# Optimization experiments

Measured on AMD Instinct MI355X. Metric: run time of the kernel, lower is better.

## Reference

```python
import jax, jax.numpy as jnp
import numpy as np

B, Himg, Wimg, C, NH = 16, 64, 64, 256, 8
HD = C // NH  # 32
N = Himg * Wimg  # 4096


def _rotations(h, w, hd):
    # RMT/RAVLT 2D axial RoPE: head_dim split into two halves (rows, cols),
    # each half holds k_max = hd//4 complex frequencies.
    k_max = hd // 4
    theta = 1.0 / (10000.0 ** (np.arange(k_max) / k_max))
    ang_h = np.arange(h)[:, None] * theta  # (h, k_max)
    ang_w = np.arange(w)[:, None] * theta  # (w, k_max)
    ang = np.concatenate([
        np.broadcast_to(ang_h[:, None, :], (h, w, k_max)),
        np.broadcast_to(ang_w[None, :, :], (h, w, k_max)),
    ], axis=-1)  # (h, w, hd//2)
    return jnp.asarray(np.cos(ang), jnp.float32), jnp.asarray(np.sin(ang), jnp.float32)

COS, SIN = _rotations(Himg, Wimg, HD)


def _rope(x):
    # x: (b, nh, H, W, hd); complex rotation of (even, odd) channel pairs
    xr, xi = x[..., 0::2], x[..., 1::2]
    out_r = xr * COS - xi * SIN
    out_i = xr * SIN + xi * COS
    return jnp.stack([out_r, out_i], axis=-1).reshape(x.shape)


def setup_inputs() -> dict:
    key = jax.random.key(0)
    ks = jax.random.split(key, 5)
    return {
        "x": jax.random.normal(ks[0], (B, N, C), jnp.float32),
        "w_qkvo": jax.random.normal(ks[1], (C, 4 * C), jnp.float32) * 0.02,
        "b_qkvo": jnp.zeros((4 * C,), jnp.float32),
        "lepe_w": jax.random.normal(ks[2], (C, 1, 5, 5), jnp.float32) * 0.02,
        "lepe_b": jnp.zeros((C,), jnp.float32),
        "w_proj": jax.random.normal(ks[3], (C, C), jnp.float32) * 0.02,
        "b_proj": jnp.zeros((C,), jnp.float32),
    }


def reference(x, w_qkvo, b_qkvo, lepe_w, lepe_b, w_proj, b_proj):
    b, n, c = x.shape
    scale = HD ** -0.5
    qkvo = x @ w_qkvo + b_qkvo  # (b, n, 4c)
    q, k, v, o = (qkvo[..., i * c:(i + 1) * c] for i in range(4))
    # LePE: depthwise 5x5 conv on v viewed as an image
    v_img = v.reshape(b, Himg, Wimg, c).transpose(0, 3, 1, 2)  # NCHW
    lepe = jax.lax.conv_general_dilated(
        v_img, lepe_w, window_strides=(1, 1), padding=[(2, 2), (2, 2)],
        dimension_numbers=("NCHW", "OIHW", "NCHW"), feature_group_count=c,
    ) + lepe_b[None, :, None, None]
    # ELU+1 feature map
    q = jax.nn.elu(q) + 1.0
    k = jax.nn.elu(k) + 1.0
    q = q.reshape(b, n, NH, HD).transpose(0, 2, 1, 3)  # (b, nh, n, hd)
    k = k.reshape(b, n, NH, HD).transpose(0, 2, 1, 3)
    v = v.reshape(b, n, NH, HD).transpose(0, 2, 1, 3)
    # efficiency reweighting of keys
    q_mean = q.mean(axis=-2, keepdims=True)  # (b, nh, 1, hd)
    eff = jax.nn.softmax(scale * jnp.einsum("bhod,bhnd->bhon", q_mean, k), axis=-1)
    k = k * eff.transpose(0, 1, 3, 2) * n  # (b, nh, n, hd)
    # RoPE on q and reweighted k
    q_rope = _rope(q.reshape(b, NH, Himg, Wimg, HD)).reshape(b, NH, n, HD)
    k_rope = _rope(k.reshape(b, NH, Himg, Wimg, HD)).reshape(b, NH, n, HD)
    # normalizer from non-rope q and mean of reweighted k
    z = 1.0 / (jnp.einsum("bhnd,bhod->bhno", q, k.mean(axis=-2, keepdims=True)) + 1e-6)
    # linear attention: kv accumulation then q @ kv (scale n^-1 split as n^-0.5 each)
    inv_sqrt_n = n ** -0.5
    kv = jnp.einsum("bhnd,bhne->bhde", k_rope * inv_sqrt_n, v * inv_sqrt_n)  # (b, nh, hd, hd)
    out = jnp.einsum("bhnd,bhde->bhne", q_rope, kv) * z
    out = out.transpose(0, 2, 1, 3).reshape(b, n, c)
    out = out + lepe.transpose(0, 2, 3, 1).reshape(b, n, c)
    out = out * o  # gate
    return out @ w_proj + b_proj
```

## Files before the change

### kernel.cpp

```cpp
#include <hip/hip_runtime.h>
#include <math.h>

constexpr int B   = 16;
constexpr int IH  = 64;
constexpr int IW  = 64;
constexpr int C   = 256;
constexpr int NH  = 8;
constexpr int HD  = 32;
constexpr int N   = IH * IW;
constexpr int C4  = 4 * C;

using f16x8 = __attribute__((ext_vector_type(8))) _Float16;
using f32x4 = __attribute__((ext_vector_type(4))) float;

__global__ void k_tables(float* __restrict__ cosT, float* __restrict__ sinT) {
  int t = blockIdx.x * 256 + threadIdx.x;
  int j = t & 15, pix = t >> 4;
  int y = pix >> 6, x = pix & 63;
  int jj = j & 7;
  double theta = pow(10000.0, -(double)jj / 8.0);
  double pos = (j < 8) ? (double)y : (double)x;
  double ang = pos * theta;
  cosT[t] = (float)cos(ang);
  sinT[t] = (float)sin(ang);
}

__global__ void k_split_wT(const float* __restrict__ w, int ldb,
                           _Float16* __restrict__ hiT, _Float16* __restrict__ loT) {
  int n = blockIdx.x;
  int k = threadIdx.x;
  float v = w[(size_t)k * ldb + n];
  _Float16 h = (_Float16)v;
  hiT[(size_t)n * 256 + k] = h;
  loT[(size_t)n * 256 + k] = (_Float16)(v - (float)h);
}

__global__ __launch_bounds__(256) void k_gemm_split(
    const float* __restrict__ A, int lda,
    const _Float16* __restrict__ BhT, const _Float16* __restrict__ BlT,
    const float* __restrict__ bias, float* __restrict__ Cm, int ldc,
    int nelu, float* __restrict__ qpart) {
  __shared__ _Float16 lds[4 * 5120];
  _Float16* AhL = lds;
  _Float16* AlL = lds + 5120;
  _Float16* BhL = lds + 10240;
  _Float16* BlL = lds + 15360;
  int t = threadIdx.x;
  int m0 = blockIdx.x * 128, n0 = blockIdx.y * 128;
  int lane = t & 63;
  int wm = t >> 7, wn = (t >> 6) & 1;
  int lr = lane & 15, lg = lane >> 4;
  int srow = t >> 1, sseg = t & 1;

  f32x4 acc[4][4] = {};

  const float* aP = &A[(size_t)(m0 + srow) * lda + sseg * 16];
  const _Float16* bhP = &BhT[(size_t)(n0 + srow) * 256 + sseg * 16];
  const _Float16* blP = &BlT[(size_t)(n0 + srow) * 256 + sseg * 16];
  float4 ar0 = *(const float4*)(aP + 0);
  float4 ar1 = *(const float4*)(aP + 4);
  float4 ar2 = *(const float4*)(aP + 8);
  float4 ar3 = *(const float4*)(aP + 12);
  f16x8 brh0 = *(const f16x8*)(bhP + 0);
  f16x8 brh1 = *(const f16x8*)(bhP + 8);
  f16x8 brl0 = *(const f16x8*)(blP + 0);
  f16x8 brl1 = *(const f16x8*)(blP + 8);

  for (int kc = 0; kc < 256; kc += 32) {
    {
      float av[16] = {ar0.x, ar0.y, ar0.z, ar0.w, ar1.x, ar1.y, ar1.z, ar1.w,
                      ar2.x, ar2.y, ar2.z, ar2.w, ar3.x, ar3.y, ar3.z, ar3.w};
      f16x8 h0, h1, l0, l1;
#pragma unroll
      for (int j = 0; j < 8; ++j) {
        _Float16 h = (_Float16)av[j];
        h0[j] = h; l0[j] = (_Float16)(av[j] - (float)h);
        _Float16 h2 = (_Float16)av[j + 8];
        h1[j] = h2; l1[j] = (_Float16)(av[j + 8] - (float)h2);
      }
      int d = srow * 40 + sseg * 16;
      *(f16x8*)&AhL[d] = h0; *(f16x8*)&AhL[d + 8] = h1;
      *(f16x8*)&AlL[d] = l0; *(f16x8*)&AlL[d + 8] = l1;
      *(f16x8*)&BhL[d] = brh0; *(f16x8*)&BhL[d + 8] = brh1;
      *(f16x8*)&BlL[d] = brl0; *(f16x8*)&BlL[d + 8] = brl1;
    }
    __syncthreads();

    if (kc + 32 < 256) {
      const float* aN = aP + kc + 32;
      const _Float16* bhN = bhP + kc + 32;
      const _Float16* blN = blP + kc + 32;
      ar0 = *(const float4*)(aN + 0);
      ar1 = *(const float4*)(aN + 4);
      ar2 = *(const float4*)(aN + 8);
      ar3 = *(const float4*)(aN + 12);
      brh0 = *(const f16x8*)(bhN + 0);
      brh1 = *(const f16x8*)(bhN + 8);
      brl0 = *(const f16x8*)(blN + 0);
      brl1 = *(const f16x8*)(blN + 8);
    }

    f16x8 ah[4], al[4];
#pragma unroll
    for (int mi = 0; mi < 4; ++mi) {
      int ar = (wm * 64 + mi * 16 + lr) * 40 + lg * 8;
      ah[mi] = *(const f16x8*)&AhL[ar];
      al[mi] = *(const f16x8*)&AlL[ar];
    }
#pragma unroll
    for (int ni = 0; ni < 4; ++ni) {
      int br = (wn * 64 + ni * 16 + lr) * 40 + lg * 8;
      f16x8 bh = *(const f16x8*)&BhL[br];
      f16x8 bl = *(const f16x8*)&BlL[br];
#pragma unroll
      for (int mi = 0; mi < 4; ++mi) {
        acc[mi][ni] = __builtin_amdgcn_mfma_f32_16x16x32_f16(ah[mi], bh, acc[mi][ni], 0, 0, 0);
        acc[mi][ni] = __builtin_amdgcn_mfma_f32_16x16x32_f16(al[mi], bh, acc[mi][ni], 0, 0, 0);
        acc[mi][ni] = __builtin_amdgcn_mfma_f32_16x16x32_f16(ah[mi], bl, acc[mi][ni], 0, 0, 0);
      }
    }
    __syncthreads();
  }

  float* Cl = reinterpret_cast<float*>(lds);
  int ri2 = t >> 3, c0 = (t & 7) << 4;
  bool doq = (qpart != nullptr) && (n0 < 256);
  float qs[16] = {};
#pragma unroll
  for (int mi = 0; mi < 4; ++mi) {
#pragma unroll
    for (int ni = 0; ni < 4; ++ni) {
      int col = wn * 64 + ni * 16 + lr;
#pragma unroll
      for (int r = 0; r < 4; ++r)
        Cl[(wm * 16 + lg * 4 + r) * 132 + col] = acc[mi][ni][r];
    }
    __syncthreads();
    int grow = m0 + (ri2 >> 4) * 64 + mi * 16 + (ri2 & 15);
#pragma unroll
    for (int j = 0; j < 4; ++j) {
      int col = n0 + c0 + j * 4;
      float4 v = *(const float4*)&Cl[ri2 * 132 + c0 + j * 4];
      float4 bb = *(const float4*)&bias[col];
      v.x += bb.x; v.y += bb.y; v.z += bb.z; v.w += bb.w;
      if (col < nelu) {
        v.x = (v.x > 0.f) ? v.x + 1.f : expf(v.x);
        v.y = (v.y > 0.f) ? v.y + 1.f : expf(v.y);
        v.z = (v.z > 0.f) ? v.z + 1.f : expf(v.z);
        v.w = (v.w > 0.f) ? v.w + 1.f : expf(v.w);
      }
      if (doq) {
        qs[j * 4 + 0] += v.x; qs[j * 4 + 1] += v.y;
        qs[j * 4 + 2] += v.z; qs[j * 4 + 3] += v.w;
      }
      *(float4*)&Cm[(size_t)grow * ldc + col] = v;
    }
    __syncthreads();
  }
  if (doq) {
#pragma unroll
    for (int j = 0; j < 4; ++j) {
      float4 w4 = {qs[j*4+0], qs[j*4+1], qs[j*4+2], qs[j*4+3]};
      *(float4*)&Cl[ri2 * 132 + c0 + j * 4] = w4;
    }
    __syncthreads();
    if (t < 128) {
      float ssum = 0.f;
#pragma unroll
      for (int rr = 0; rr < 32; ++rr) ssum += Cl[rr * 132 + t];
      int b_local = m0 >> 12, rowblk = (m0 >> 7) & 31;
      qpart[(size_t)(b_local * 32 + rowblk) * 256 + n0 + t] = ssum;
    }
  }
}

__global__ __launch_bounds__(256) void k_kvflash(
    const float* __restrict__ qkvo, const float* __restrict__ qpart,
    const float* __restrict__ cosT, const float* __restrict__ sinT,
    float* __restrict__ kvp) {
  __shared__ float qm[32];
  __shared__ float sL[512];
  __shared__ float red[256];
  __shared__ float ktG[4][32][36];
  __shared__ float vtG[4][32][36];
  int bh = blockIdx.x, chunk = blockIdx.y;
  int b = bh >> 3, h = bh & 7;
  int t = threadIdx.x;
  int nbase = chunk << 9;

  if (t < 32) {
    float s = 0.f;
#pragma unroll
    for (int rb = 0; rb < 32; ++rb)
      s += qpart[(size_t)(b * 32 + rb) * 256 + (h << 5) + t];
    qm[t] = s * (1.0f / N) * 0.1767766952966369f;
  }
  __syncthreads();

  float qmr[32];
#pragma unroll
  for (int i = 0; i < 32; ++i) qmr[i] = qm[i];
  float mx = -3.4e38f;
#pragma unroll
  for (int i = 0; i < 2; ++i) {
    int n = nbase + t + i * 256;
    const float* kp = &qkvo[(size_t)(b * N + n) * C4 + 256 + (h << 5)];
    float dot = 0.f;
#pragma unroll
    for (int j = 0; j < 8; ++j) {
      float4 k4 = *(const float4*)(kp + (j << 2));
      dot += k4.x * qmr[j*4] + k4.y * qmr[j*4+1] + k4.z * qmr[j*4+2] + k4.w * qmr[j*4+3];
    }
    sL[t + i * 256] = dot;
    mx = fmaxf(mx, dot);
  }
  red[t] = mx; __syncthreads();
  for (int off = 128; off > 0; off >>= 1) {
    if (t < off) red[t] = fmaxf(red[t], red[t + off]);
    __syncthreads();
  }
  float mx_c = red[0];
  __syncthreads();
  float psum = expf(sL[t] - mx_c) + expf(sL[t + 256] - mx_c);
  red[t] = psum; __syncthreads();
  for (int off = 128; off > 0; off >>= 1) {
    if (t < off) red[t] += red[t + off];
    __syncthreads();
  }
  float sum_c = red[0];

  int sg = t >> 6;
  int lane = t & 63;
  int d0 = (lane >> 3) << 2;
  int e0 = (lane & 7) << 2;
  int srow_l = (t >> 1) & 31;
  int sdh = t & 1;
  float acc[4][4] = {};
  float km16[16] = {};

  for (int s = 0; s < 4; ++s) {
    int nloc = sg * 128 + s * 32 + srow_l;
    int n = nbase + nloc;
    const float* kp = &qkvo[(size_t)(b * N + n) * C4 + 256 + (h << 5) + sdh * 16];
    const float* vp = kp + 256;
    float ef = expf(sL[nloc] - mx_c);
    float kl[16], vl[16];
#pragma unroll
    for (int j4 = 0; j4 < 4; ++j4) {
      float4 k4 = *(const float4*)(kp + (j4 << 2));
      float4 v4 = *(const float4*)(vp + (j4 << 2));
      k4.x *= ef; k4.y *= ef; k4.z *= ef; k4.w *= ef;
      km16[j4*4+0] += k4.x; km16[j4*4+1] += k4.y;
      km16[j4*4+2] += k4.z; km16[j4*4+3] += k4.w;
      kl[j4*4+0] = k4.x; kl[j4*4+1] = k4.y; kl[j4*4+2] = k4.z; kl[j4*4+3] = k4.w;
      vl[j4*4+0] = v4.x; vl[j4*4+1] = v4.y; vl[j4*4+2] = v4.z; vl[j4*4+3] = v4.w;
    }
#pragma unroll
    for (int p = 0; p < 8; ++p) {
      float cc = cosT[(n << 4) + sdh * 8 + p];
      float sn = sinT[(n << 4) + sdh * 8 + p];
      float kr = kl[2*p], ki = kl[2*p+1];
      kl[2*p]   = kr * cc - ki * sn;
      kl[2*p+1] = kr * sn + ki * cc;
    }
#pragma unroll
    for (int j4 = 0; j4 < 4; ++j4) {
      float4 kw = {kl[j4*4+0], kl[j4*4+1], kl[j4*4+2], kl[j4*4+3]};
      float4 vw = {vl[j4*4+0], vl[j4*4+1], vl[j4*4+2], vl[j4*4+3]};
      *(float4*)&ktG[sg][srow_l][sdh*16 + (j4 << 2)] = kw;
      *(float4*)&vtG[sg][srow_l][sdh*16 + (j4 << 2)] = vw;
    }
    __syncthreads();
    __builtin_amdgcn_s_setprio(1);
#pragma unroll
    for (int nn = 0; nn < 32; ++nn) {
      float4 k4 = *(const float4*)&ktG[sg][nn][d0];
      float4 v4 = *(const float4*)&vtG[sg][nn][e0];
      float kv_[4] = {k4.x, k4.y, k4.z, k4.w};
      float vv_[4] = {v4.x, v4.y, v4.z, v4.w};
#pragma unroll
      for (int i = 0; i < 4; ++i)
#pragma unroll
        for (int j = 0; j < 4; ++j)
          acc[i][j] = fmaf(kv_[i], vv_[j], acc[i][j]);
    }
    __builtin_amdgcn_s_setprio(0);
    __syncthreads();
  }

  float* mrg = &ktG[0][0][0];
#pragma unroll
  for (int i = 0; i < 4; ++i)
#pragma unroll
    for (int j = 0; j < 4; ++j)
      mrg[sg * 1024 + (d0 + i) * 32 + (e0 + j)] = acc[i][j];
  __syncthreads();
  size_t o = (size_t)(bh * 8 + chunk) * 1058;
  {
    int idx = t << 2;
    float4 r;
    r.x = mrg[idx+0] + mrg[1024+idx+0] + mrg[2048+idx+0] + mrg[3072+idx+0];
    r.y = mrg[idx+1] + mrg[1024+idx+1] + mrg[2048+idx+1] + mrg[3072+idx+1];
    r.z = mrg[idx+2] + mrg[1024+idx+2] + mrg[2048+idx+2] + mrg[3072+idx+2];
    r.w = mrg[idx+3] + mrg[1024+idx+3] + mrg[2048+idx+3] + mrg[3072+idx+3];
    kvp[o + idx + 0] = r.x; kvp[o + idx + 1] = r.y;
    kvp[o + idx + 2] = r.z; kvp[o + idx + 3] = r.w;
  }
  float* kmb = &vtG[0][0][0];
#pragma unroll
  for (int j = 0; j < 16; ++j) kmb[t * 16 + j] = km16[j];
  __syncthreads();
  if (t < 32) {
    int dh = t >> 4, dj = t & 15;
    float ssum = 0.f;
    for (int r = 0; r < 128; ++r) ssum += kmb[((r << 1) + dh) * 16 + dj];
    kvp[o + 1024 + t] = ssum;
  }
  if (t == 0) {
    kvp[o + 1056] = mx_c;
    kvp[o + 1057] = sum_c;
  }
}

__global__ __launch_bounds__(256) void k_kvfinal(
    const float* __restrict__ kvp, float* __restrict__ kvkm) {
  __shared__ float fc[8];
  int bh = blockIdx.x;
  int t = threadIdx.x;
  if (t == 0) {
    float mxs[8], sums[8];
    float mx = -3.4e38f;
#pragma unroll
    for (int c = 0; c < 8; ++c) {
      size_t o = (size_t)(bh * 8 + c) * 1058;
      mxs[c] = kvp[o + 1056];
      sums[c] = kvp[o + 1057];
      mx = fmaxf(mx, mxs[c]);
    }
    float T = 0.f;
#pragma unroll
    for (int c = 0; c < 8; ++c) T += sums[c] * expf(mxs[c] - mx);
    float invT = 1.0f / T;
#pragma unroll
    for (int c = 0; c < 8; ++c) fc[c] = expf(mxs[c] - mx) * invT;
  }
  __syncthreads();
  float f0 = fc[0], f1 = fc[1], f2 = fc[2], f3 = fc[3];
  float f4 = fc[4], f5 = fc[5], f6 = fc[6], f7 = fc[7];
  for (int j = t; j < 1056; j += 256) {
    size_t o = (size_t)(bh * 8) * 1058 + j;
    float v = kvp[o] * f0 + kvp[o + 1058] * f1 + kvp[o + 2 * 1058] * f2 +
              kvp[o + 3 * 1058] * f3 + kvp[o + 4 * 1058] * f4 +
              kvp[o + 5 * 1058] * f5 + kvp[o + 6 * 1058] * f6 +
              kvp[o + 7 * 1058] * f7;
    kvkm[(size_t)bh * 1056 + j] = v;
  }
}

__global__ __launch_bounds__(256) void k_lepe(
    const float* __restrict__ qkvo, const float* __restrict__ wgt,
    const float* __restrict__ lb, float* __restrict__ lepe_out, int b0) {
  int blk = blockIdx.x;
  int b = blk >> 8, rem = blk & 255;
  int y = rem >> 2, x0 = (rem & 3) << 4;
  int c = threadIdx.x;
  float w[25];
#pragma unroll
  for (int i = 0; i < 25; ++i) w[i] = wgt[c * 25 + i];
  float bias = lb[c];
  float acc[16];
#pragma unroll
  for (int p = 0; p < 16; ++p) acc[p] = bias;
#pragma unroll
  for (int dy = 0; dy < 5; ++dy) {
    int yy = y + dy - 2;
    if (yy < 0 || yy >= IH) continue;
    size_t rowb = (size_t)(b * N + (yy << 6)) * C4 + 512 + c;
#pragma unroll
    for (int dx = 0; dx < 5; ++dx) {
      float wv = w[dy * 5 + dx];
#pragma unroll
      for (int p = 0; p < 16; ++p) {
        int xx = x0 + p + dx - 2;
        if (xx < 0 || xx >= IW) continue;
        acc[p] = fmaf(qkvo[rowb + (size_t)xx * C4], wv, acc[p]);
      }
    }
  }
#pragma unroll
  for (int p = 0; p < 16; ++p)
    lepe_out[(size_t)((b0 + b) * N + (y << 6) + x0 + p) * C + c] = acc[p];
}

__global__ __launch_bounds__(256) void k_out_combine(
    float* __restrict__ qkvo, const float* __restrict__ kvkm,
    const float* __restrict__ cosT, const float* __restrict__ sinT,
    const float* __restrict__ lepe, int b0) {
  __shared__ float kvs[1024];
  __shared__ float kms[32];
  int bh = blockIdx.x, chunk = blockIdx.y;
  int b = bh >> 3, h = bh & 7;
  int t = threadIdx.x;
  reinterpret_cast<float4*>(kvs)[t] =
      reinterpret_cast<const float4*>(&kvkm[(size_t)bh * 1056])[t];
  if (t < 32) kms[t] = kvkm[(size_t)bh * 1056 + 1024 + t];
  __syncthreads();
  int n = (chunk << 8) + t;
  size_t rowbase = (size_t)(b * N + n) * C4;
  float q[32];
#pragma unroll
  for (int i = 0; i < 8; ++i) {
    float4 q4 = *reinterpret_cast<const float4*>(&qkvo[rowbase + (h << 5) + (i << 2)]);
    q[i * 4 + 0] = q4.x; q[i * 4 + 1] = q4.y; q[i * 4 + 2] = q4.z; q[i * 4 + 3] = q4.w;
  }
  float dot = 0.f;
#pragma unroll
  for (int dd = 0; dd < 32; ++dd) dot += q[dd] * kms[dd];
  float zv = 1.0f / (dot + 1e-6f);
  const float* cp = &cosT[n << 4];
  const float* sp = &sinT[n << 4];
#pragma unroll
  for (int j = 0; j < 16; ++j) {
    float cc = cp[j], ss = sp[j];
    float qr = q[2 * j], qi = q[2 * j + 1];
    q[2 * j]     = qr * cc - qi * ss;
    q[2 * j + 1] = qr * ss + qi * cc;
  }
  size_t oc = (size_t)((b0 + b) * N + n) * C + (h << 5);
#pragma unroll
  for (int e4 = 0; e4 < 8; ++e4) {
    float ax = 0, ay = 0, az = 0, aw = 0;
#pragma unroll
    for (int dd = 0; dd < 32; ++dd) {
      float4 kv4 = *reinterpret_cast<const float4*>(&kvs[(dd << 5) + (e4 << 2)]);
      float qd = q[dd];
      ax = fmaf(qd, kv4.x, ax); ay = fmaf(qd, kv4.y, ay);
      az = fmaf(qd, kv4.z, az); aw = fmaf(qd, kv4.w, aw);
    }
    float4 lp = *reinterpret_cast<const float4*>(&lepe[oc + (e4 << 2)]);
    float4 ov = *reinterpret_cast<const float4*>(
        &qkvo[rowbase + 768 + (h << 5) + (e4 << 2)]);
    float4 r;
    r.x = (ax * zv + lp.x) * ov.x;
    r.y = (ay * zv + lp.y) * ov.y;
    r.z = (az * zv + lp.z) * ov.z;
    r.w = (aw * zv + lp.w) * ov.w;
    *reinterpret_cast<float4*>(&qkvo[rowbase + (h << 5) + (e4 << 2)]) = r;
  }
}

static inline size_t ws_bytes_needed(int bpp) {
  size_t pn = (size_t)bpp * N;
  size_t f32c = pn * C4
              + (size_t)bpp * 32 * 256
              + (size_t)bpp * NH * 8 * 1058
              + (size_t)bpp * NH * 1056
              + (size_t)N * 16 * 2;
  size_t f16c = (size_t)C * C4 * 2
              + (size_t)C * C * 2;
  return f32c * 4 + f16c * 2;
}

extern "C" void kernel_launch(void* const* d_in, const int* in_sizes, int n_in,
                              void* d_out, int out_size, void* d_ws, size_t ws_size,
                              hipStream_t stream) {
  const float* x      = (const float*)d_in[0];
  const float* w_qkvo = (const float*)d_in[1];
  const float* b_qkvo = (const float*)d_in[2];
  const float* lepe_w = (const float*)d_in[3];
  const float* lepe_b = (const float*)d_in[4];
  const float* w_proj = (const float*)d_in[5];
  const float* b_proj = (const float*)d_in[6];
  float* out = (float*)d_out;
  float* ws  = (float*)d_ws;

  int bpp = 2;
  if (ws_bytes_needed(16) <= ws_size) bpp = 16;
  else if (ws_bytes_needed(8) <= ws_size) bpp = 8;
  else if (ws_bytes_needed(4) <= ws_size) bpp = 4;

  size_t pn = (size_t)bpp * N;
  int nbh = bpp * NH;
  float* qkvo  = ws;
  float* qpart = qkvo  + pn * C4;
  float* kvp   = qpart + (size_t)bpp * 32 * 256;
  float* kvkm  = kvp   + (size_t)nbh * 8 * 1058;
  float* cosT  = kvkm  + (size_t)nbh * 1056;
  float* sinT  = cosT  + (size_t)N * 16;
  _Float16* wqh = (_Float16*)(sinT + (size_t)N * 16);
  _Float16* wql = wqh + (size_t)C * C4;
  _Float16* wph = wql + (size_t)C * C4;
  _Float16* wpl = wph + (size_t)C * C;

  k_tables<<<N * 16 / 256, 256, 0, stream>>>(cosT, sinT);
  k_split_wT<<<C4, 256, 0, stream>>>(w_qkvo, C4, wqh, wql);
  k_split_wT<<<C, 256, 0, stream>>>(w_proj, C, wph, wpl);

  for (int b0 = 0; b0 < B; b0 += bpp) {
    k_gemm_split<<<dim3(pn / 128, C4 / 128), 256, 0, stream>>>(
        x + (size_t)b0 * N * C, C, wqh, wql, b_qkvo, qkvo, C4, 512, qpart);
    k_kvflash<<<dim3(nbh, 8), 256, 0, stream>>>(qkvo, qpart, cosT, sinT, kvp);
    k_kvfinal<<<nbh, 256, 0, stream>>>(kvp, kvkm);
    k_lepe<<<bpp * IH * 4, 256, 0, stream>>>(qkvo, lepe_w, lepe_b, out, b0);
    k_out_combine<<<dim3(nbh, 16), 256, 0, stream>>>(qkvo, kvkm, cosT, sinT, out, b0);
    k_gemm_split<<<dim3(pn / 128, C / 128), 256, 0, stream>>>(
        qkvo, C4, wph, wpl, b_proj, out + (size_t)b0 * N * C, C, 0, nullptr);
  }
}
```

Measured before the change: 539.8 us.

## Fuse kv chunk merge into output combine and double-buffer GEMM A loads

Removes the separate k_kvfinal kernel. Each k_out_combine block now computes the softmax chunk weights and merges the eight partial kv/kmean chunks itself, using vectorized float4 loads with a padded 1060-float stride. Separately, the split-fp16 GEMM keeps two A register stages so global loads run two k-steps ahead, and the k loop is fully unrolled. In exchange, the merge is recomputed redundantly by all 16 chunk blocks per head, and the extra A stage raises register pressure.

```diff
diff --git a/kernel.cpp b/kernel.cpp
--- a/kernel.cpp
+++ b/kernel.cpp
@@ -9,6 +9,7 @@
 constexpr int HD  = 32;
 constexpr int N   = IH * IW;
 constexpr int C4  = 4 * C;
+constexpr int KVP_STRIDE = 1060;
 
 using f16x8 = __attribute__((ext_vector_type(8))) _Float16;
 using f32x4 = __attribute__((ext_vector_type(4))) float;
@@ -57,19 +58,28 @@
   const float* aP = &A[(size_t)(m0 + srow) * lda + sseg * 16];
   const _Float16* bhP = &BhT[(size_t)(n0 + srow) * 256 + sseg * 16];
   const _Float16* blP = &BlT[(size_t)(n0 + srow) * 256 + sseg * 16];
-  float4 ar0 = *(const float4*)(aP + 0);
-  float4 ar1 = *(const float4*)(aP + 4);
-  float4 ar2 = *(const float4*)(aP + 8);
-  float4 ar3 = *(const float4*)(aP + 12);
+
+  float4 areg[2][4];
+#pragma unroll
+  for (int j = 0; j < 4; ++j) areg[0][j] = *(const float4*)(aP + (j << 2));
+#pragma unroll
+  for (int j = 0; j < 4; ++j) areg[1][j] = *(const float4*)(aP + 32 + (j << 2));
   f16x8 brh0 = *(const f16x8*)(bhP + 0);
   f16x8 brh1 = *(const f16x8*)(bhP + 8);
   f16x8 brl0 = *(const f16x8*)(blP + 0);
   f16x8 brl1 = *(const f16x8*)(blP + 8);
 
-  for (int kc = 0; kc < 256; kc += 32) {
+#pragma unroll
+  for (int it = 0; it < 8; ++it) {
+    const int kc = it * 32;
+    const int cur = it & 1;
     {
-      float av[16] = {ar0.x, ar0.y, ar0.z, ar0.w, ar1.x, ar1.y, ar1.z, ar1.w,
-                      ar2.x, ar2.y, ar2.z, ar2.w, ar3.x, ar3.y, ar3.z, ar3.w};
+      float av[16];
+#pragma unroll
+      for (int j = 0; j < 4; ++j) {
+        av[j * 4 + 0] = areg[cur][j].x; av[j * 4 + 1] = areg[cur][j].y;
+        av[j * 4 + 2] = areg[cur][j].z; av[j * 4 + 3] = areg[cur][j].w;
+      }
       f16x8 h0, h1, l0, l1;
 #pragma unroll
       for (int j = 0; j < 8; ++j) {
@@ -86,18 +96,16 @@
     }
     __syncthreads();
 
-    if (kc + 32 < 256) {
-      const float* aN = aP + kc + 32;
-      const _Float16* bhN = bhP + kc + 32;
-      const _Float16* blN = blP + kc + 32;
-      ar0 = *(const float4*)(aN + 0);
-      ar1 = *(const float4*)(aN + 4);
-      ar2 = *(const float4*)(aN + 8);
-      ar3 = *(const float4*)(aN + 12);
-      brh0 = *(const f16x8*)(bhN + 0);
-      brh1 = *(const f16x8*)(bhN + 8);
-      brl0 = *(const f16x8*)(blN + 0);
-      brl1 = *(const f16x8*)(blN + 8);
+    if (it < 6) {
+#pragma unroll
+      for (int j = 0; j < 4; ++j)
+        areg[cur][j] = *(const float4*)(aP + kc + 64 + (j << 2));
+    }
+    if (it < 7) {
+      brh0 = *(const f16x8*)(bhP + kc + 32);
+      brh1 = *(const f16x8*)(bhP + kc + 40);
+      brl0 = *(const f16x8*)(blP + kc + 32);
+      brl1 = *(const f16x8*)(blP + kc + 40);
     }
 
     f16x8 ah[4], al[4];
@@ -295,7 +303,7 @@
     for (int j = 0; j < 4; ++j)
       mrg[sg * 1024 + (d0 + i) * 32 + (e0 + j)] = acc[i][j];
   __syncthreads();
-  size_t o = (size_t)(bh * 8 + chunk) * 1058;
+  size_t o = (size_t)(bh * 8 + chunk) * KVP_STRIDE;
   {
     int idx = t << 2;
     float4 r;
@@ -322,41 +330,6 @@
   }
 }
 
-__global__ __launch_bounds__(256) void k_kvfinal(
-    const float* __restrict__ kvp, float* __restrict__ kvkm) {
-  __shared__ float fc[8];
-  int bh = blockIdx.x;
-  int t = threadIdx.x;
-  if (t == 0) {
-    float mxs[8], sums[8];
-    float mx = -3.4e38f;
-#pragma unroll
-    for (int c = 0; c < 8; ++c) {
-      size_t o = (size_t)(bh * 8 + c) * 1058;
-      mxs[c] = kvp[o + 1056];
-      sums[c] = kvp[o + 1057];
-      mx = fmaxf(mx, mxs[c]);
-    }
-    float T = 0.f;
-#pragma unroll
-    for (int c = 0; c < 8; ++c) T += sums[c] * expf(mxs[c] - mx);
-    float invT = 1.0f / T;
-#pragma unroll
-    for (int c = 0; c < 8; ++c) fc[c] = expf(mxs[c] - mx) * invT;
-  }
-  __syncthreads();
-  float f0 = fc[0], f1 = fc[1], f2 = fc[2], f3 = fc[3];
-  float f4 = fc[4], f5 = fc[5], f6 = fc[6], f7 = fc[7];
-  for (int j = t; j < 1056; j += 256) {
-    size_t o = (size_t)(bh * 8) * 1058 + j;
-    float v = kvp[o] * f0 + kvp[o + 1058] * f1 + kvp[o + 2 * 1058] * f2 +
-              kvp[o + 3 * 1058] * f3 + kvp[o + 4 * 1058] * f4 +
-              kvp[o + 5 * 1058] * f5 + kvp[o + 6 * 1058] * f6 +
-              kvp[o + 7 * 1058] * f7;
-    kvkm[(size_t)bh * 1056 + j] = v;
-  }
-}
-
 __global__ __launch_bounds__(256) void k_lepe(
     const float* __restrict__ qkvo, const float* __restrict__ wgt,
     const float* __restrict__ lb, float* __restrict__ lepe_out, int b0) {
@@ -393,17 +366,52 @@
 }
 
 __global__ __launch_bounds__(256) void k_out_combine(
-    float* __restrict__ qkvo, const float* __restrict__ kvkm,
+    float* __restrict__ qkvo, const float* __restrict__ kvp,
     const float* __restrict__ cosT, const float* __restrict__ sinT,
     const float* __restrict__ lepe, int b0) {
   __shared__ float kvs[1024];
   __shared__ float kms[32];
+  __shared__ float fcs[8];
   int bh = blockIdx.x, chunk = blockIdx.y;
   int b = bh >> 3, h = bh & 7;
   int t = threadIdx.x;
-  reinterpret_cast<float4*>(kvs)[t] =
-      reinterpret_cast<const float4*>(&kvkm[(size_t)bh * 1056])[t];
-  if (t < 32) kms[t] = kvkm[(size_t)bh * 1056 + 1024 + t];
+  if (t == 0) {
+    float mxs[8], sums[8];
+    float mx = -3.4e38f;
+#pragma unroll
+    for (int c = 0; c < 8; ++c) {
+      size_t o = (size_t)(bh * 8 + c) * KVP_STRIDE;
+      mxs[c] = kvp[o + 1056];
+      sums[c] = kvp[o + 1057];
+      mx = fmaxf(mx, mxs[c]);
+    }
+    float T = 0.f;
+#pragma unroll
+    for (int c = 0; c < 8; ++c) T += sums[c] * expf(mxs[c] - mx);
+    float invT = 1.0f / T;
+#pragma unroll
+    for (int c = 0; c < 8; ++c) fcs[c] = expf(mxs[c] - mx) * invT;
+  }
+  __syncthreads();
+  {
+    int idx = t << 2;
+    size_t o0 = (size_t)(bh * 8) * KVP_STRIDE + idx;
+    float4 r = {0.f, 0.f, 0.f, 0.f};
+#pragma unroll
+    for (int c = 0; c < 8; ++c) {
+      float4 p = *(const float4*)&kvp[o0 + (size_t)c * KVP_STRIDE];
+      float f = fcs[c];
+      r.x += p.x * f; r.y += p.y * f; r.z += p.z * f; r.w += p.w * f;
+    }
+    *(float4*)&kvs[idx] = r;
+    if (t < 32) {
+      float s = 0.f;
+#pragma unroll
+      for (int c = 0; c < 8; ++c)
+        s += kvp[(size_t)(bh * 8 + c) * KVP_STRIDE + 1024 + t] * fcs[c];
+      kms[t] = s;
+    }
+  }
   __syncthreads();
   int n = (chunk << 8) + t;
   size_t rowbase = (size_t)(b * N + n) * C4;
@@ -453,8 +461,7 @@
   size_t pn = (size_t)bpp * N;
   size_t f32c = pn * C4
               + (size_t)bpp * 32 * 256
-              + (size_t)bpp * NH * 8 * 1058
-              + (size_t)bpp * NH * 1056
+              + (size_t)bpp * NH * 8 * KVP_STRIDE
               + (size_t)N * 16 * 2;
   size_t f16c = (size_t)C * C4 * 2
               + (size_t)C * C * 2;
@@ -484,8 +491,7 @@
   float* qkvo  = ws;
   float* qpart = qkvo  + pn * C4;
   float* kvp   = qpart + (size_t)bpp * 32 * 256;
-  float* kvkm  = kvp   + (size_t)nbh * 8 * 1058;
-  float* cosT  = kvkm  + (size_t)nbh * 1056;
+  float* cosT  = kvp   + (size_t)nbh * 8 * KVP_STRIDE;
   float* sinT  = cosT  + (size_t)N * 16;
   _Float16* wqh = (_Float16*)(sinT + (size_t)N * 16);
   _Float16* wql = wqh + (size_t)C * C4;
@@ -500,9 +506,8 @@
     k_gemm_split<<<dim3(pn / 128, C4 / 128), 256, 0, stream>>>(
         x + (size_t)b0 * N * C, C, wqh, wql, b_qkvo, qkvo, C4, 512, qpart);
     k_kvflash<<<dim3(nbh, 8), 256, 0, stream>>>(qkvo, qpart, cosT, sinT, kvp);
-    k_kvfinal<<<nbh, 256, 0, stream>>>(kvp, kvkm);
     k_lepe<<<bpp * IH * 4, 256, 0, stream>>>(qkvo, lepe_w, lepe_b, out, b0);
-    k_out_combine<<<dim3(nbh, 16), 256, 0, stream>>>(qkvo, kvkm, cosT, sinT, out, b0);
+    k_out_combine<<<dim3(nbh, 16), 256, 0, stream>>>(qkvo, kvp, cosT, sinT, out, b0);
     k_gemm_split<<<dim3(pn / 128, C / 128), 256, 0, stream>>>(
         qkvo, C4, wph, wpl, b_proj, out + (size_t)b0 * N * C, C, 0, nullptr);
   }
```

Measured after the change: 550.3 us. About the same (+1.9%).
